# Performance work log

Hardware: AMD Instinct MI355X
Metric: run time of the kernel (lower is better)

Reference implementation:

```python
import jax, jax.numpy as jnp
import numpy as np

N = 50000       # nodes
E = 1600000     # edges (before self-loops)
NFEAT = 256
NHID = 8        # hidden units per head
HEADS = 8
NCLASS = 16
L1 = 0.5        # damping lambda layer 1
L2 = 0.5        # damping lambda layer 2
SLOPE = 0.2     # LeakyReLU negative slope (PyG GATConv default)


def setup_inputs() -> dict:
    ks = jax.random.split(jax.random.key(0), 16)
    g = lambda k, shape, fan: jax.random.normal(k, shape, jnp.float32) * (1.0 / np.sqrt(fan))
    return {
        "x": jax.random.normal(ks[0], (N, NFEAT), jnp.float32),
        "edge_index": jax.random.randint(ks[1], (2, E), 0, N, jnp.int64),
        # conv1: GATConv(nfeat -> nhid, heads=HEADS, concat=True)
        "W1": g(ks[2], (NFEAT, HEADS * NHID), NFEAT),
        "a1_src": g(ks[3], (HEADS, NHID), NHID),
        "a1_dst": g(ks[4], (HEADS, NHID), NHID),
        "b1": jnp.zeros((HEADS * NHID,), jnp.float32),
        # conv2: GATConv(nhid*heads -> nclass, heads=1, concat=False)
        "W2": g(ks[5], (HEADS * NHID, NCLASS), HEADS * NHID),
        "a2_src": g(ks[6], (1, NCLASS), NCLASS),
        "a2_dst": g(ks[7], (1, NCLASS), NCLASS),
        "b2": jnp.zeros((NCLASS,), jnp.float32),
        # side-branch linear layers
        "fc1_W": g(ks[8], (NFEAT, NHID), NFEAT),
        "fc1_b": jnp.zeros((NHID,), jnp.float32),
        "fc2_W": g(ks[9], (HEADS * NHID, NCLASS), HEADS * NHID),
        "fc2_b": jnp.zeros((NCLASS,), jnp.float32),
    }


def gat_conv(x, W, a_src, a_dst, b, src, dst, heads, outc, concat):
    n = x.shape[0]
    h = (x @ W).reshape(n, heads, outc)                 # [N, H, C]
    alpha_s = jnp.sum(h * a_src, axis=-1)               # [N, H]
    alpha_d = jnp.sum(h * a_dst, axis=-1)               # [N, H]
    e = jax.nn.leaky_relu(alpha_s[src] + alpha_d[dst], SLOPE)  # [Etot, H]
    # segment softmax over incoming edges of each destination node
    m = jax.ops.segment_max(e, dst, num_segments=n)
    m = jax.lax.stop_gradient(m)                        # max-shift is grad-neutral
    ex = jnp.exp(e - m[dst])
    denom = jax.ops.segment_sum(ex, dst, num_segments=n)
    alpha = ex / denom[dst]                             # [Etot, H]
    out = jax.ops.segment_sum(h[src] * alpha[:, :, None], dst, num_segments=n)
    if concat:
        out = out.reshape(n, heads * outc)
    else:
        out = out.mean(axis=1)
    return out + b


def reference(x, edge_index, W1, a1_src, a1_dst, b1, W2, a2_src, a2_dst, b2,
              fc1_W, fc1_b, fc2_W, fc2_b):
    loop = jnp.arange(N, dtype=edge_index.dtype)
    src = jnp.concatenate([edge_index[0], loop])
    dst = jnp.concatenate([edge_index[1], loop])
    # layer 1: GATConv + damped linear side branch
    out1 = gat_conv(x, W1, a1_src, a1_dst, b1, src, dst, HEADS, NHID, True)
    side1 = jnp.tile(x @ fc1_W + fc1_b, (1, HEADS))     # cat of heads copies
    h = jax.nn.elu(out1 - L1 * side1)                   # [N, H*C]
    # layer 2
    out2 = gat_conv(h, W2, a2_src, a2_dst, b2, src, dst, 1, NCLASS, False)
    side2 = h @ fc2_W + fc2_b
    return jax.nn.log_softmax(out2 - L2 * side2, axis=1)
```

## Files before the change

kernel.cpp:

```cpp
#include <hip/hip_runtime.h>
#include <hip/hip_bf16.h>
#include <cstddef>

constexpr int N      = 50000;
constexpr int E      = 1600000;
constexpr int NFEAT  = 256;
constexpr float SLOPE = 0.2f;
constexpr float L1d  = 0.5f;
constexpr float L2d  = 0.5f;

constexpr int BSHIFT = 7;
constexpr int NBUK   = (N + 127) >> BSHIFT;
constexpr int EPB    = 4096;
constexpr int NBLK   = (E + EPB - 1) / EPB;
constexpr int CAP    = 5120;

constexpr size_t al64(size_t x) { return (x + 63) & ~size_t(63); }
constexpr size_t W_OFFS  = 0;
constexpr size_t W_CSR   = W_OFFS  + al64(N + 1);
constexpr size_t W_STAGE = W_CSR   + (size_t)E;
constexpr size_t W_BHIST = W_STAGE + (size_t)E;
constexpr size_t W_TOT   = W_BHIST + al64((size_t)NBLK * NBUK);
constexpr size_t W_BBASE = W_TOT   + al64(NBUK);
constexpr size_t W_H1B   = W_BBASE + al64(NBUK + 1);
constexpr size_t W_S1B   = W_H1B   + (size_t)N * 32;
constexpr size_t W_D1    = W_S1B   + (size_t)N * 4;
constexpr size_t W_SIDE1 = W_D1    + (size_t)N * 8;
constexpr size_t W_HF    = W_SIDE1 + (size_t)N * 8;
constexpr size_t W_H2B   = W_HF    + (size_t)N * 64;
constexpr size_t W_SIDE2 = W_H2B   + (size_t)N * 8;
constexpr size_t W_S2B   = W_SIDE2 + (size_t)N * 16;
constexpr size_t W_D2    = W_S2B   + al64(N / 2);

typedef short bf16x8 __attribute__((ext_vector_type(8)));
typedef float f32x4  __attribute__((ext_vector_type(4)));

__device__ inline short f2bf(float f) {
    unsigned u = __builtin_bit_cast(unsigned, f);
    u += 0x7FFF + ((u >> 16) & 1);
    return (short)(u >> 16);
}


__global__ __launch_bounds__(256) void p1_hist_kernel(const int* __restrict__ ei,
                                                      int* __restrict__ bhist) {
    __shared__ int hist[NBUK];
    int tid = threadIdx.x;
    for (int j = tid; j < NBUK; j += 256) hist[j] = 0;
    __syncthreads();
    int base = blockIdx.x * EPB;
    int end = base + EPB; if (end > E) end = E;
    for (int i = base + tid; i < end; i += 256) {
        int d = ei[E + i];
        atomicAdd(&hist[d >> BSHIFT], 1);
    }
    __syncthreads();
    for (int j = tid; j < NBUK; j += 256) bhist[(size_t)blockIdx.x * NBUK + j] = hist[j];
}

__global__ __launch_bounds__(512) void s1_scan_kernel(int* __restrict__ bhist,
                                                      int* __restrict__ tot) {
    __shared__ int sd[512];
    int tid = threadIdx.x;
    int b = blockIdx.x;
    int v = (tid < NBLK) ? bhist[(size_t)tid * NBUK + b] : 0;
    sd[tid] = v;
    __syncthreads();
    for (int off = 1; off < 512; off <<= 1) {
        int t = (tid >= off) ? sd[tid - off] : 0;
        __syncthreads();
        sd[tid] += t;
        __syncthreads();
    }
    if (tid < NBLK) bhist[(size_t)tid * NBUK + b] = sd[tid] - v;
    if (tid == 511) tot[b] = sd[511];
}

__global__ __launch_bounds__(512) void s2_scan_kernel(const int* __restrict__ tot,
                                                      int* __restrict__ bbase,
                                                      int* __restrict__ offs) {
    __shared__ int sd[512];
    int tid = threadIdx.x;
    int v = (tid < NBUK) ? tot[tid] : 0;
    sd[tid] = v;
    __syncthreads();
    for (int off = 1; off < 512; off <<= 1) {
        int t = (tid >= off) ? sd[tid - off] : 0;
        __syncthreads();
        sd[tid] += t;
        __syncthreads();
    }
    if (tid < NBUK) bbase[tid] = sd[tid] - v;
    if (tid == 0) { bbase[NBUK] = E; offs[N] = E; }
}

__global__ __launch_bounds__(256) void p2_stage_kernel(const int* __restrict__ ei,
                                                       const int* __restrict__ bhist,
                                                       const int* __restrict__ bbase,
                                                       unsigned int* __restrict__ stage) {
    __shared__ int cur[NBUK];
    int tid = threadIdx.x;
    for (int j = tid; j < NBUK; j += 256)
        cur[j] = bbase[j] + bhist[(size_t)blockIdx.x * NBUK + j];
    __syncthreads();
    int base = blockIdx.x * EPB;
    int end = base + EPB; if (end > E) end = E;
    for (int i = base + tid; i < end; i += 256) {
        int s = ei[i];
        int d = ei[E + i];
        int b = d >> BSHIFT;
        int pos = atomicAdd(&cur[b], 1);
        stage[pos] = ((unsigned int)(d & 127) << 24) | (unsigned int)s;
    }
}

__global__ __launch_bounds__(256) void p3_fine_kernel(const unsigned int* __restrict__ stage,
                                                      const int* __restrict__ bbase,
                                                      int* __restrict__ offs,
                                                      int* __restrict__ csr) {
    __shared__ unsigned int sstage[CAP];
    __shared__ int hist[128];
    __shared__ int scn[128];
    __shared__ int cur[128];
    int tid = threadIdx.x;
    int b = blockIdx.x;
    int ebase = bbase[b], eend = bbase[b + 1];
    int cnt = eend - ebase;
    if (tid < 128) hist[tid] = 0;
    __syncthreads();
    for (int i = tid; i < cnt; i += 256) {
        unsigned int p = stage[ebase + i];
        if (i < CAP) sstage[i] = p;
        atomicAdd(&hist[p >> 24], 1);
    }
    __syncthreads();
    if (tid < 128) scn[tid] = hist[tid];
    __syncthreads();
    for (int off = 1; off < 128; off <<= 1) {
        int t = (tid < 128 && tid >= off) ? scn[tid - off] : 0;
        __syncthreads();
        if (tid < 128) scn[tid] += t;
        __syncthreads();
    }
    if (tid < 128) {
        int excl = scn[tid] - hist[tid];
        cur[tid] = excl;
        int v = (b << BSHIFT) + tid;
        if (v < N) offs[v] = ebase + excl;
    }
    __syncthreads();
    for (int i = tid; i < cnt; i += 256) {
        unsigned int p = (i < CAP) ? sstage[i] : stage[ebase + i];
        int dloc = (int)(p >> 24);
        int s = (int)(p & 0xFFFFFFu);
        int r = atomicAdd(&cur[dloc], 1);
        csr[ebase + r] = s;
    }
}

__global__ __launch_bounds__(256) void gemm1_kernel(const float* __restrict__ x,
                                                    const float* __restrict__ W1,
                                                    const float* __restrict__ fc1W,
                                                    const float* __restrict__ fc1b,
                                                    short* __restrict__ h1b,
                                                    float* __restrict__ side1) {
    __shared__ bf16x8 wfrag[2560];
    int tid = threadIdx.x;

    for (int s = tid; s < 2560; s += 256) {
        int l = s & 63;
        int t = s >> 6;
        int nt = t % 5, kt = t / 5;
        int col = nt * 16 + (l & 15);
        int kbase = kt * 32 + (l >> 4) * 8;
        bf16x8 v;
#pragma unroll
        for (int j = 0; j < 8; ++j) {
            float f = 0.f;
            if (col < 64)      f = W1[(size_t)(kbase + j) * 64 + col];
            else if (col < 72) f = fc1W[(size_t)(kbase + j) * 8 + (col - 64)];
            v[j] = f2bf(f);
        }
        wfrag[s] = v;
    }
    __syncthreads();

    int w = tid >> 6;
    int l = tid & 63;
    int row0 = blockIdx.x * 64;
    int arow = row0 + w * 16 + (l & 15);
    if (arow >= N) arow = N - 1;
    const float* ap = x + (size_t)arow * NFEAT + ((l >> 4) * 8);

    f32x4 acc[5];
#pragma unroll
    for (int nt = 0; nt < 5; ++nt) acc[nt] = (f32x4){0.f, 0.f, 0.f, 0.f};

#pragma unroll
    for (int kt = 0; kt < 8; ++kt) {
        float4 alo = *reinterpret_cast<const float4*>(ap + kt * 32);
        float4 ahi = *reinterpret_cast<const float4*>(ap + kt * 32 + 4);
        bf16x8 af;
        af[0] = f2bf(alo.x); af[1] = f2bf(alo.y); af[2] = f2bf(alo.z); af[3] = f2bf(alo.w);
        af[4] = f2bf(ahi.x); af[5] = f2bf(ahi.y); af[6] = f2bf(ahi.z); af[7] = f2bf(ahi.w);
#pragma unroll
        for (int nt = 0; nt < 5; ++nt) {
            acc[nt] = __builtin_amdgcn_mfma_f32_16x16x32_bf16(
                af, wfrag[(kt * 5 + nt) * 64 + l], acc[nt], 0, 0, 0);
        }
    }

    int cbase = l & 15;
    int rbase = row0 + w * 16 + (l >> 4) * 4;
#pragma unroll
    for (int nt = 0; nt < 4; ++nt) {
#pragma unroll
        for (int r = 0; r < 4; ++r) {
            int row = rbase + r;
            if (row < N) h1b[(size_t)row * 64 + nt * 16 + cbase] = f2bf(acc[nt][r]);
        }
    }
    if (cbase < 8) {
        float bb = fc1b[cbase];
#pragma unroll
        for (int r = 0; r < 4; ++r) {
            int row = rbase + r;
            if (row < N) side1[(size_t)row * 8 + cbase] = acc[4][r] + bb;
        }
    }
}

__global__ __launch_bounds__(256) void alpha1_kernel(const __hip_bfloat16* __restrict__ h1b,
                                                     const float* __restrict__ a1s,
                                                     const float* __restrict__ a1d,
                                                     __hip_bfloat16* __restrict__ s1b,
                                                     float* __restrict__ d1) {
    int wave = threadIdx.x >> 6;
    int lane = threadIdx.x & 63;
    int v = blockIdx.x * 4 + wave;
    if (v >= N) return;
    float hv = __bfloat162float(h1b[(size_t)v * 64 + lane]);
    float sa = hv * a1s[lane];
    float sd = hv * a1d[lane];
#pragma unroll
    for (int off = 1; off < 8; off <<= 1) {
        sa += __shfl_xor(sa, off, 64);
        sd += __shfl_xor(sd, off, 64);
    }
    if ((lane & 7) == 0) {
        s1b[v * 8 + (lane >> 3)] = __float2bfloat16(sa);
        d1[v * 8 + (lane >> 3)] = sd;
    }
}

__global__ __launch_bounds__(256) void agg1_kernel(const int* __restrict__ offs,
                                                   const int* __restrict__ csr,
                                                   const __hip_bfloat16* __restrict__ h1b,
                                                   const __hip_bfloat16* __restrict__ s1b,
                                                   const float* __restrict__ d1,
                                                   const float* __restrict__ side1,
                                                   const float* __restrict__ b1,
                                                   float* __restrict__ hf) {
    int wave = threadIdx.x >> 6;
    int lane = threadIdx.x & 63;
    int v = blockIdx.x * 4 + wave;
    if (v >= N) return;
    int j  = lane >> 3;
    int hh = lane & 7;
    int hc = lane >> 3;

    float dv_att = d1[v * 8 + hh];
    float dv_ch  = __shfl(dv_att, hc, 64);

    float e0 = __bfloat162float(s1b[v * 8 + hc]) + dv_ch;
    e0 = fmaxf(e0, SLOPE * e0);
    float ex0 = __expf(e0);
    float acc = ex0 * __bfloat162float(h1b[(size_t)v * 64 + lane]);
    float den_ch = ex0;
    float den_att = 0.f;

    int beg = offs[v], end = offs[v + 1];
    int nfull = (end - beg) >> 3;
    int i = beg;
    for (int g = 0; g < nfull; ++g, i += 8) {
        int s = csr[i + j];
        float a = __bfloat162float(s1b[s * 8 + hh]) + dv_att;
        a = fmaxf(a, SLOPE * a);
        float xv = __expf(a);
        den_att += xv;
#pragma unroll
        for (int jj = 0; jj < 8; ++jj) {
            int sj = __builtin_amdgcn_readlane(s, jj * 8);
            float xj = __shfl(xv, jj * 8 + hc, 64);
            const __hip_bfloat16* hp = h1b + ((size_t)sj << 6);
            acc += xj * __bfloat162float(hp[lane]);
        }
    }
    for (; i < end; ++i) {
        int s = csr[i];
        float a = __bfloat162float(s1b[s * 8 + hc]) + dv_ch;
        a = fmaxf(a, SLOPE * a);
        float x = __expf(a);
        acc += x * __bfloat162float(h1b[(size_t)s * 64 + lane]);
        den_ch += x;
    }

    den_att += __shfl_xor(den_att, 8, 64);
    den_att += __shfl_xor(den_att, 16, 64);
    den_att += __shfl_xor(den_att, 32, 64);
    float den = den_ch + __shfl(den_att, hc, 64);

    float o = acc / den + b1[lane];
    float z = o - L1d * side1[v * 8 + (lane & 7)];
    hf[(size_t)v * 64 + lane] = z > 0.f ? z : (__expf(z) - 1.f);
}

__global__ __launch_bounds__(256) void gemm2_kernel(const float* __restrict__ hf,
                                                    const float* __restrict__ W2,
                                                    const float* __restrict__ fc2W,
                                                    const float* __restrict__ fc2b,
                                                    __hip_bfloat16* __restrict__ h2b,
                                                    float* __restrict__ side2) {
    __shared__ float xs[128][65];
    __shared__ float ws[64][33];
    int tid = threadIdx.x;
    int ty = tid >> 3;
    int tx = tid & 7;
    int row0 = blockIdx.x * 128;

    float acc[4][4];
#pragma unroll
    for (int i = 0; i < 4; ++i)
#pragma unroll
        for (int j = 0; j < 4; ++j) acc[i][j] = 0.f;

    int lr = tid >> 4;
    int lj = tid & 15;
#pragma unroll
    for (int it = 0; it < 8; ++it) {
        int r = lr + it * 16;
        int grow = row0 + r;
        if (grow >= N) grow = N - 1;
        float4 vv = *reinterpret_cast<const float4*>(&hf[(size_t)grow * 64 + lj * 4]);
        xs[r][lj * 4 + 0] = vv.x;
        xs[r][lj * 4 + 1] = vv.y;
        xs[r][lj * 4 + 2] = vv.z;
        xs[r][lj * 4 + 3] = vv.w;
    }
    for (int idx = tid; idx < 64 * 32; idx += 256) {
        int k = idx >> 5;
        int c = idx & 31;
        float v = (c < 16) ? W2[(size_t)k * 16 + c] : fc2W[(size_t)k * 16 + (c - 16)];
        ws[k][c] = v;
    }
    __syncthreads();
#pragma unroll 4
    for (int k = 0; k < 64; ++k) {
        float xv[4], wv[4];
#pragma unroll
        for (int i = 0; i < 4; ++i) xv[i] = xs[ty * 4 + i][k];
#pragma unroll
        for (int j = 0; j < 4; ++j) wv[j] = ws[k][tx * 4 + j];
#pragma unroll
        for (int i = 0; i < 4; ++i)
#pragma unroll
            for (int j = 0; j < 4; ++j) acc[i][j] += xv[i] * wv[j];
    }

#pragma unroll
    for (int i = 0; i < 4; ++i) {
        int row = row0 + ty * 4 + i;
        if (row >= N) continue;
#pragma unroll
        for (int j = 0; j < 4; ++j) {
            int c = tx * 4 + j;
            if (c < 16) h2b[(size_t)row * 16 + c] = __float2bfloat16(acc[i][j]);
            else        side2[(size_t)row * 16 + (c - 16)] = acc[i][j] + fc2b[c - 16];
        }
    }
}

__global__ __launch_bounds__(256) void alpha2_kernel(const __hip_bfloat16* __restrict__ h2b,
                                                     const float* __restrict__ a2s,
                                                     const float* __restrict__ a2d,
                                                     __hip_bfloat16* __restrict__ s2b,
                                                     float* __restrict__ d2) {
    int wave = threadIdx.x >> 6;
    int lane = threadIdx.x & 63;
    int vbase = (blockIdx.x * 4 + wave) * 4;
    int r = lane >> 4;
    int c = lane & 15;
    int v = vbase + r;
    float hv = (v < N) ? __bfloat162float(h2b[(size_t)v * 16 + c]) : 0.f;
    float sa = hv * a2s[c];
    float sd = hv * a2d[c];
#pragma unroll
    for (int off = 1; off < 16; off <<= 1) {
        sa += __shfl_xor(sa, off, 64);
        sd += __shfl_xor(sd, off, 64);
    }
    if (v < N && c == 0) {
        s2b[v] = __float2bfloat16(sa);
        d2[v] = sd;
    }
}

__global__ __launch_bounds__(256) void agg2_kernel(const int* __restrict__ offs,
                                                   const int* __restrict__ csr,
                                                   const __hip_bfloat16* __restrict__ h2b,
                                                   const __hip_bfloat16* __restrict__ s2b,
                                                   const float* __restrict__ d2,
                                                   const float* __restrict__ side2,
                                                   const float* __restrict__ b2,
                                                   float* __restrict__ out) {
    int wave = threadIdx.x >> 6;
    int lane = threadIdx.x & 63;
    int v = blockIdx.x * 4 + wave;
    if (v >= N) return;
    int c = lane & 15;
    int slot = lane >> 4;
    float dv = d2[v];

    float acc = 0.f, den = 0.f;
    if (slot == 0) {
        float e = __bfloat162float(s2b[v]) + dv;
        e = e > 0.f ? e : SLOPE * e;
        float ex = __expf(e);
        acc = ex * __bfloat162float(h2b[(size_t)v * 16 + c]);
        den = ex;
    }
    int beg = offs[v], end = offs[v + 1];
    int i = beg + slot;
    for (; i + 4 < end; i += 8) {
        int sA = csr[i];
        int sB = csr[i + 4];
        float aA = __bfloat162float(s2b[sA]);
        float aB = __bfloat162float(s2b[sB]);
        float hA = __bfloat162float(h2b[(size_t)sA * 16 + c]);
        float hB = __bfloat162float(h2b[(size_t)sB * 16 + c]);
        aA += dv; aA = aA > 0.f ? aA : SLOPE * aA; float xA = __expf(aA);
        aB += dv; aB = aB > 0.f ? aB : SLOPE * aB; float xB = __expf(aB);
        acc += xA * hA; den += xA;
        acc += xB * hB; den += xB;
    }
    if (i < end) {
        int s = csr[i];
        float a = __bfloat162float(s2b[s]) + dv;
        a = a > 0.f ? a : SLOPE * a;
        float x = __expf(a);
        acc += x * __bfloat162float(h2b[(size_t)s * 16 + c]);
        den += x;
    }
    acc += __shfl_xor(acc, 16, 64);
    acc += __shfl_xor(acc, 32, 64);
    den += __shfl_xor(den, 16, 64);
    den += __shfl_xor(den, 32, 64);

    float o = acc / den + b2[c];
    float z = o - L2d * side2[(size_t)v * 16 + c];

    float m = z;
#pragma unroll
    for (int off = 1; off < 16; off <<= 1) m = fmaxf(m, __shfl_xor(m, off, 64));
    float ex = __expf(z - m);
    float s = ex;
#pragma unroll
    for (int off = 1; off < 16; off <<= 1) s += __shfl_xor(s, off, 64);
    float lsm = z - m - __logf(s);
    if (slot == 0) out[(size_t)v * 16 + c] = lsm;
}

extern "C" void kernel_launch(void* const* d_in, const int* in_sizes, int n_in,
                              void* d_out, int out_size, void* d_ws, size_t ws_size,
                              hipStream_t stream) {
    const float* x    = (const float*)d_in[0];
    const int*   ei   = (const int*)d_in[1];
    const float* W1   = (const float*)d_in[2];
    const float* a1s  = (const float*)d_in[3];
    const float* a1d  = (const float*)d_in[4];
    const float* b1   = (const float*)d_in[5];
    const float* W2   = (const float*)d_in[6];
    const float* a2s  = (const float*)d_in[7];
    const float* a2d  = (const float*)d_in[8];
    const float* b2   = (const float*)d_in[9];
    const float* fc1W = (const float*)d_in[10];
    const float* fc1b = (const float*)d_in[11];
    const float* fc2W = (const float*)d_in[12];
    const float* fc2b = (const float*)d_in[13];
    float* out = (float*)d_out;

    int*   wsi = (int*)d_ws;
    float* wsf = (float*)d_ws;
    int*   offs   = wsi + W_OFFS;
    int*   csr    = wsi + W_CSR;
    unsigned int* stage = (unsigned int*)(wsi + W_STAGE);
    int*   bhist  = wsi + W_BHIST;
    int*   tot    = wsi + W_TOT;
    int*   bbase  = wsi + W_BBASE;
    __hip_bfloat16* h1b = (__hip_bfloat16*)(wsf + W_H1B);
    __hip_bfloat16* s1b = (__hip_bfloat16*)(wsf + W_S1B);
    float* d1     = wsf + W_D1;
    float* side1  = wsf + W_SIDE1;
    float* hf     = wsf + W_HF;
    __hip_bfloat16* h2b = (__hip_bfloat16*)(wsf + W_H2B);
    float* side2  = wsf + W_SIDE2;
    __hip_bfloat16* s2b = (__hip_bfloat16*)(wsf + W_S2B);
    float* d2     = wsf + W_D2;

    p1_hist_kernel<<<NBLK, 256, 0, stream>>>(ei, bhist);
    s1_scan_kernel<<<NBUK, 512, 0, stream>>>(bhist, tot);
    s2_scan_kernel<<<1, 512, 0, stream>>>(tot, bbase, offs);
    p2_stage_kernel<<<NBLK, 256, 0, stream>>>(ei, bhist, bbase, stage);
    p3_fine_kernel<<<NBUK, 256, 0, stream>>>(stage, bbase, offs, csr);

    gemm1_kernel<<<(N + 63) / 64, 256, 0, stream>>>(x, W1, fc1W, fc1b,
                                                    (short*)h1b, side1);
    alpha1_kernel<<<(N + 3) / 4, 256, 0, stream>>>(h1b, a1s, a1d, s1b, d1);
    agg1_kernel<<<(N + 3) / 4, 256, 0, stream>>>(offs, csr, h1b, s1b, d1, side1, b1, hf);

    gemm2_kernel<<<(N + 127) / 128, 256, 0, stream>>>(hf, W2, fc2W, fc2b, h2b, side2);
    alpha2_kernel<<<(N + 15) / 16, 256, 0, stream>>>(h2b, a2s, a2d, s2b, d2);
    agg2_kernel<<<(N + 3) / 4, 256, 0, stream>>>(offs, csr, h2b, s2b, d2, side2, b2, out);
}
```

Before: 171.8 us.

## Software-pipeline neighbor gathers in both aggregation kernels with clamped masked groups

Result: faster. 156.7 us (-8.8%).

```diff
diff --git a/kernel.cpp b/kernel.cpp
--- a/kernel.cpp
+++ b/kernel.cpp
@@ -41,6 +41,10 @@
     return (short)(u >> 16);
 }
 
+__device__ inline float bfu2f(unsigned short u) {
+    return __builtin_bit_cast(float, (unsigned)u << 16);
+}
+
 
 __global__ __launch_bounds__(256) void p1_hist_kernel(const int* __restrict__ ei,
                                                       int* __restrict__ bhist) {
@@ -255,8 +259,8 @@
 
 __global__ __launch_bounds__(256) void agg1_kernel(const int* __restrict__ offs,
                                                    const int* __restrict__ csr,
-                                                   const __hip_bfloat16* __restrict__ h1b,
-                                                   const __hip_bfloat16* __restrict__ s1b,
+                                                   const unsigned short* __restrict__ h1u,
+                                                   const unsigned short* __restrict__ s1u,
                                                    const float* __restrict__ d1,
                                                    const float* __restrict__ side1,
                                                    const float* __restrict__ b1,
@@ -272,43 +276,102 @@
     float dv_att = d1[v * 8 + hh];
     float dv_ch  = __shfl(dv_att, hc, 64);
 
-    float e0 = __bfloat162float(s1b[v * 8 + hc]) + dv_ch;
+    float e0 = bfu2f(s1u[v * 8 + hc]) + dv_ch;
     e0 = fmaxf(e0, SLOPE * e0);
     float ex0 = __expf(e0);
-    float acc = ex0 * __bfloat162float(h1b[(size_t)v * 64 + lane]);
-    float den_ch = ex0;
+    float acc = ex0 * bfu2f(h1u[(size_t)v * 64 + lane]);
+    float den0 = ex0;
     float den_att = 0.f;
 
     int beg = offs[v], end = offs[v + 1];
-    int nfull = (end - beg) >> 3;
-    int i = beg;
-    for (int g = 0; g < nfull; ++g, i += 8) {
-        int s = csr[i + j];
-        float a = __bfloat162float(s1b[s * 8 + hh]) + dv_att;
+    int deg = end - beg;
+    int ng = (deg + 7) >> 3;
+
+    auto csrg = [&](int g) {
+        int idx = beg + g * 8 + j;
+        idx = idx < end - 1 ? idx : end - 1;
+        idx = idx > 0 ? idx : 0;
+        return csr[idx];
+    };
+
+    unsigned short hA[8], hB[8];
+    int sA = 0, sB = 0;
+    float svA = 0.f, svB = 0.f;
+
+    if (ng > 0) {
+        sA = csrg(0);
+        svA = bfu2f(s1u[sA * 8 + hh]);
+#pragma unroll
+        for (int jj = 0; jj < 8; ++jj) {
+            int sj = __builtin_amdgcn_readlane(sA, jj * 8);
+            const unsigned short* p = h1u + ((size_t)sj << 6);
+            hA[jj] = p[lane];
+        }
+        sB = csrg(1);
+    }
+
+    int g = 0;
+    for (; g + 1 < ng; g += 2) {
+        svB = bfu2f(s1u[sB * 8 + hh]);
+#pragma unroll
+        for (int jj = 0; jj < 8; ++jj) {
+            int sj = __builtin_amdgcn_readlane(sB, jj * 8);
+            const unsigned short* p = h1u + ((size_t)sj << 6);
+            hB[jj] = p[lane];
+        }
+        int sC = csrg(g + 2);
+        {
+            float a = svA + dv_att;
+            a = fmaxf(a, SLOPE * a);
+            float xv = __expf(a);
+            xv = (beg + g * 8 + j < end) ? xv : 0.f;
+            den_att += xv;
+#pragma unroll
+            for (int jj = 0; jj < 8; ++jj) {
+                float xj = __shfl(xv, jj * 8 + hc, 64);
+                acc += xj * bfu2f(hA[jj]);
+            }
+        }
+        sA = sC;
+        svA = bfu2f(s1u[sA * 8 + hh]);
+#pragma unroll
+        for (int jj = 0; jj < 8; ++jj) {
+            int sj = __builtin_amdgcn_readlane(sA, jj * 8);
+            const unsigned short* p = h1u + ((size_t)sj << 6);
+            hA[jj] = p[lane];
+        }
+        int sD = csrg(g + 3);
+        {
+            float a = svB + dv_att;
+            a = fmaxf(a, SLOPE * a);
+            float xv = __expf(a);
+            xv = (beg + (g + 1) * 8 + j < end) ? xv : 0.f;
+            den_att += xv;
+#pragma unroll
+            for (int jj = 0; jj < 8; ++jj) {
+                float xj = __shfl(xv, jj * 8 + hc, 64);
+                acc += xj * bfu2f(hB[jj]);
+            }
+        }
+        sB = sD;
+    }
+    if (g < ng) {
+        float a = svA + dv_att;
         a = fmaxf(a, SLOPE * a);
         float xv = __expf(a);
+        xv = (beg + g * 8 + j < end) ? xv : 0.f;
         den_att += xv;
 #pragma unroll
         for (int jj = 0; jj < 8; ++jj) {
-            int sj = __builtin_amdgcn_readlane(s, jj * 8);
             float xj = __shfl(xv, jj * 8 + hc, 64);
-            const __hip_bfloat16* hp = h1b + ((size_t)sj << 6);
-            acc += xj * __bfloat162float(hp[lane]);
-        }
-    }
-    for (; i < end; ++i) {
-        int s = csr[i];
-        float a = __bfloat162float(s1b[s * 8 + hc]) + dv_ch;
-        a = fmaxf(a, SLOPE * a);
-        float x = __expf(a);
-        acc += x * __bfloat162float(h1b[(size_t)s * 64 + lane]);
-        den_ch += x;
+            acc += xj * bfu2f(hA[jj]);
+        }
     }
 
     den_att += __shfl_xor(den_att, 8, 64);
     den_att += __shfl_xor(den_att, 16, 64);
     den_att += __shfl_xor(den_att, 32, 64);
-    float den = den_ch + __shfl(den_att, hc, 64);
+    float den = den0 + __shfl(den_att, hc, 64);
 
     float o = acc / den + b1[lane];
     float z = o - L1d * side1[v * 8 + (lane & 7)];
@@ -407,8 +470,8 @@
 
 __global__ __launch_bounds__(256) void agg2_kernel(const int* __restrict__ offs,
                                                    const int* __restrict__ csr,
-                                                   const __hip_bfloat16* __restrict__ h2b,
-                                                   const __hip_bfloat16* __restrict__ s2b,
+                                                   const unsigned short* __restrict__ h2u,
+                                                   const unsigned short* __restrict__ s2u,
                                                    const float* __restrict__ d2,
                                                    const float* __restrict__ side2,
                                                    const float* __restrict__ b2,
@@ -423,34 +486,67 @@
 
     float acc = 0.f, den = 0.f;
     if (slot == 0) {
-        float e = __bfloat162float(s2b[v]) + dv;
-        e = e > 0.f ? e : SLOPE * e;
+        float e = bfu2f(s2u[v]) + dv;
+        e = fmaxf(e, SLOPE * e);
         float ex = __expf(e);
-        acc = ex * __bfloat162float(h2b[(size_t)v * 16 + c]);
+        acc = ex * bfu2f(h2u[(size_t)v * 16 + c]);
         den = ex;
     }
     int beg = offs[v], end = offs[v + 1];
-    int i = beg + slot;
-    for (; i + 4 < end; i += 8) {
-        int sA = csr[i];
-        int sB = csr[i + 4];
-        float aA = __bfloat162float(s2b[sA]);
-        float aB = __bfloat162float(s2b[sB]);
-        float hA = __bfloat162float(h2b[(size_t)sA * 16 + c]);
-        float hB = __bfloat162float(h2b[(size_t)sB * 16 + c]);
-        aA += dv; aA = aA > 0.f ? aA : SLOPE * aA; float xA = __expf(aA);
-        aB += dv; aB = aB > 0.f ? aB : SLOPE * aB; float xB = __expf(aB);
-        acc += xA * hA; den += xA;
-        acc += xB * hB; den += xB;
-    }
-    if (i < end) {
-        int s = csr[i];
-        float a = __bfloat162float(s2b[s]) + dv;
-        a = a > 0.f ? a : SLOPE * a;
+    int deg = end - beg;
+    int ng = (deg + 3) >> 2;
+
+    auto csrg = [&](int g) {
+        int idx = beg + g * 4 + slot;
+        idx = idx < end - 1 ? idx : end - 1;
+        idx = idx > 0 ? idx : 0;
+        return csr[idx];
+    };
+
+    int sA = 0, sB = 0;
+    float svA = 0.f, svB = 0.f, hvA = 0.f, hvB = 0.f;
+    if (ng > 0) {
+        sA = csrg(0);
+        svA = bfu2f(s2u[sA]);
+        hvA = bfu2f(h2u[(size_t)sA * 16 + c]);
+        sB = csrg(1);
+    }
+    int g = 0;
+    for (; g + 1 < ng; g += 2) {
+        svB = bfu2f(s2u[sB]);
+        hvB = bfu2f(h2u[(size_t)sB * 16 + c]);
+        int sC = csrg(g + 2);
+        {
+            float a = svA + dv;
+            a = fmaxf(a, SLOPE * a);
+            float x = __expf(a);
+            x = (beg + g * 4 + slot < end) ? x : 0.f;
+            acc += x * hvA;
+            den += x;
+        }
+        sA = sC;
+        svA = bfu2f(s2u[sA]);
+        hvA = bfu2f(h2u[(size_t)sA * 16 + c]);
+        int sD = csrg(g + 3);
+        {
+            float a = svB + dv;
+            a = fmaxf(a, SLOPE * a);
+            float x = __expf(a);
+            x = (beg + (g + 1) * 4 + slot < end) ? x : 0.f;
+            acc += x * hvB;
+            den += x;
+        }
+        sB = sD;
+    }
+    if (g < ng) {
+        float a = svA + dv;
+        a = fmaxf(a, SLOPE * a);
         float x = __expf(a);
-        acc += x * __bfloat162float(h2b[(size_t)s * 16 + c]);
+        x = (beg + g * 4 + slot < end) ? x : 0.f;
+        acc += x * hvA;
         den += x;
     }
+
     acc += __shfl_xor(acc, 16, 64);
     acc += __shfl_xor(acc, 32, 64);
     den += __shfl_xor(den, 16, 64);
@@ -516,9 +612,15 @@
     gemm1_kernel<<<(N + 63) / 64, 256, 0, stream>>>(x, W1, fc1W, fc1b,
                                                     (short*)h1b, side1);
     alpha1_kernel<<<(N + 3) / 4, 256, 0, stream>>>(h1b, a1s, a1d, s1b, d1);
-    agg1_kernel<<<(N + 3) / 4, 256, 0, stream>>>(offs, csr, h1b, s1b, d1, side1, b1, hf);
+    agg1_kernel<<<(N + 3) / 4, 256, 0, stream>>>(offs, csr,
+                                                 (const unsigned short*)h1b,
+                                                 (const unsigned short*)s1b,
+                                                 d1, side1, b1, hf);
 
     gemm2_kernel<<<(N + 127) / 128, 256, 0, stream>>>(hf, W2, fc2W, fc2b, h2b, side2);
     alpha2_kernel<<<(N + 15) / 16, 256, 0, stream>>>(h2b, a2s, a2d, s2b, d2);
-    agg2_kernel<<<(N + 3) / 4, 256, 0, stream>>>(offs, csr, h2b, s2b, d2, side2, b2, out);
-}
+    agg2_kernel<<<(N + 3) / 4, 256, 0, stream>>>(offs, csr,
+                                                 (const unsigned short*)h2b,
+                                                 (const unsigned short*)s2b,
+                                                 d2, side2, b2, out);
+}
```

## Software-pipeline neighbor gathers in both aggregation kernels with swizzle-based broadcasts

Applied to the files above, without the earlier changes.

After: 171.0 us. Within noise of the previous version (-0.4%).

```diff
diff --git a/kernel.cpp b/kernel.cpp
--- a/kernel.cpp
+++ b/kernel.cpp
@@ -41,6 +41,12 @@
     return (short)(u >> 16);
 }
 
+__device__ inline float bfu2f(unsigned short u) {
+    return __builtin_bit_cast(float, (unsigned)u << 16);
+}
+
+#define SWZ8(x, PAT) __builtin_bit_cast(float, __builtin_amdgcn_ds_swizzle(__builtin_bit_cast(int, (x)), (PAT)))
+
 
 __global__ __launch_bounds__(256) void p1_hist_kernel(const int* __restrict__ ei,
                                                       int* __restrict__ bhist) {
@@ -255,63 +261,127 @@
 
 __global__ __launch_bounds__(256) void agg1_kernel(const int* __restrict__ offs,
                                                    const int* __restrict__ csr,
-                                                   const __hip_bfloat16* __restrict__ h1b,
-                                                   const __hip_bfloat16* __restrict__ s1b,
+                                                   const unsigned short* __restrict__ h1u,
+                                                   const unsigned short* __restrict__ s1u,
                                                    const float* __restrict__ d1,
                                                    const float* __restrict__ side1,
                                                    const float* __restrict__ b1,
                                                    float* __restrict__ hf) {
-    int wave = threadIdx.x >> 6;
     int lane = threadIdx.x & 63;
-    int v = blockIdx.x * 4 + wave;
+    int v = blockIdx.x * 4 + (threadIdx.x >> 6);
     if (v >= N) return;
-    int j  = lane >> 3;
-    int hh = lane & 7;
-    int hc = lane >> 3;
-
-    float dv_att = d1[v * 8 + hh];
-    float dv_ch  = __shfl(dv_att, hc, 64);
-
-    float e0 = __bfloat162float(s1b[v * 8 + hc]) + dv_ch;
+    int j  = lane & 7;
+    int hh = lane >> 3;
+
+    float dv = d1[v * 8 + hh];
+
+    float e0 = bfu2f(s1u[v * 8 + hh]) + dv;
     e0 = fmaxf(e0, SLOPE * e0);
     float ex0 = __expf(e0);
-    float acc = ex0 * __bfloat162float(h1b[(size_t)v * 64 + lane]);
-    float den_ch = ex0;
+    float acc = ex0 * bfu2f(h1u[(size_t)v * 64 + lane]);
+    float den0 = ex0;
     float den_att = 0.f;
 
     int beg = offs[v], end = offs[v + 1];
-    int nfull = (end - beg) >> 3;
-    int i = beg;
-    for (int g = 0; g < nfull; ++g, i += 8) {
-        int s = csr[i + j];
-        float a = __bfloat162float(s1b[s * 8 + hh]) + dv_att;
+    int deg = end - beg;
+    int ngf = deg >> 3;
+    int rem = deg & 7;
+
+    const int* cb = csr + beg;
+
+    unsigned short hA[8], hB[8];
+    int s8A = 0, s8B = 0;
+    float svA = 0.f, svB = 0.f;
+
+#define LOADH(s8, h)                                                        \
+    do {                                                                     \
+        int sj0 = __builtin_amdgcn_readlane(s8, 0);                          \
+        int sj1 = __builtin_amdgcn_readlane(s8, 1);                          \
+        int sj2 = __builtin_amdgcn_readlane(s8, 2);                          \
+        int sj3 = __builtin_amdgcn_readlane(s8, 3);                          \
+        int sj4 = __builtin_amdgcn_readlane(s8, 4);                          \
+        int sj5 = __builtin_amdgcn_readlane(s8, 5);                          \
+        int sj6 = __builtin_amdgcn_readlane(s8, 6);                          \
+        int sj7 = __builtin_amdgcn_readlane(s8, 7);                          \
+        h[0] = h1u[((size_t)sj0 << 6) + lane];                               \
+        h[1] = h1u[((size_t)sj1 << 6) + lane];                               \
+        h[2] = h1u[((size_t)sj2 << 6) + lane];                               \
+        h[3] = h1u[((size_t)sj3 << 6) + lane];                               \
+        h[4] = h1u[((size_t)sj4 << 6) + lane];                               \
+        h[5] = h1u[((size_t)sj5 << 6) + lane];                               \
+        h[6] = h1u[((size_t)sj6 << 6) + lane];                               \
+        h[7] = h1u[((size_t)sj7 << 6) + lane];                               \
+    } while (0)
+
+#define COMP(sv, h)                                                          \
+    do {                                                                     \
+        float a = (sv) + dv;                                                 \
+        a = fmaxf(a, SLOPE * a);                                             \
+        float xv = __expf(a);                                                \
+        den_att += xv;                                                       \
+        acc += SWZ8(xv, 0x018) * bfu2f(h[0]);                                \
+        acc += SWZ8(xv, 0x038) * bfu2f(h[1]);                                \
+        acc += SWZ8(xv, 0x058) * bfu2f(h[2]);                                \
+        acc += SWZ8(xv, 0x078) * bfu2f(h[3]);                                \
+        acc += SWZ8(xv, 0x098) * bfu2f(h[4]);                                \
+        acc += SWZ8(xv, 0x0B8) * bfu2f(h[5]);                                \
+        acc += SWZ8(xv, 0x0D8) * bfu2f(h[6]);                                \
+        acc += SWZ8(xv, 0x0F8) * bfu2f(h[7]);                                \
+    } while (0)
+
+    if (ngf > 0) {
+        s8A = cb[j];
+        svA = bfu2f(s1u[s8A * 8 + hh]);
+        LOADH(s8A, hA);
+        if (ngf > 1) s8B = cb[8 + j];
+    }
+    int g = 0;
+    for (; g + 1 < ngf; g += 2) {
+        svB = bfu2f(s1u[s8B * 8 + hh]);
+        LOADH(s8B, hB);
+        int s8C = (g + 2 < ngf) ? cb[(g + 2) * 8 + j] : 0;
+        COMP(svA, hA);
+        s8A = s8C;
+        if (g + 2 < ngf) {
+            svA = bfu2f(s1u[s8A * 8 + hh]);
+            LOADH(s8A, hA);
+        }
+        int s8D = (g + 3 < ngf) ? cb[(g + 3) * 8 + j] : 0;
+        COMP(svB, hB);
+        s8B = s8D;
+    }
+    if (g < ngf) COMP(svA, hA);
+
+    if (rem) {
+        int idx = beg + ngf * 8 + j;
+        idx = idx < end ? idx : end - 1;
+        int s8 = csr[idx];
+        float a = bfu2f(s1u[s8 * 8 + hh]) + dv;
         a = fmaxf(a, SLOPE * a);
         float xv = __expf(a);
+        xv = (j < rem) ? xv : 0.f;
         den_att += xv;
-#pragma unroll
-        for (int jj = 0; jj < 8; ++jj) {
-            int sj = __builtin_amdgcn_readlane(s, jj * 8);
-            float xj = __shfl(xv, jj * 8 + hc, 64);
-            const __hip_bfloat16* hp = h1b + ((size_t)sj << 6);
-            acc += xj * __bfloat162float(hp[lane]);
-        }
-    }
-    for (; i < end; ++i) {
-        int s = csr[i];
-        float a = __bfloat162float(s1b[s * 8 + hc]) + dv_ch;
-        a = fmaxf(a, SLOPE * a);
-        float x = __expf(a);
-        acc += x * __bfloat162float(h1b[(size_t)s * 64 + lane]);
-        den_ch += x;
-    }
-
-    den_att += __shfl_xor(den_att, 8, 64);
-    den_att += __shfl_xor(den_att, 16, 64);
-    den_att += __shfl_xor(den_att, 32, 64);
-    float den = den_ch + __shfl(den_att, hc, 64);
+        unsigned short ht[8];
+        LOADH(s8, ht);
+        acc += SWZ8(xv, 0x018) * bfu2f(ht[0]);
+        acc += SWZ8(xv, 0x038) * bfu2f(ht[1]);
+        acc += SWZ8(xv, 0x058) * bfu2f(ht[2]);
+        acc += SWZ8(xv, 0x078) * bfu2f(ht[3]);
+        acc += SWZ8(xv, 0x098) * bfu2f(ht[4]);
+        acc += SWZ8(xv, 0x0B8) * bfu2f(ht[5]);
+        acc += SWZ8(xv, 0x0D8) * bfu2f(ht[6]);
+        acc += SWZ8(xv, 0x0F8) * bfu2f(ht[7]);
+    }
+#undef LOADH
+#undef COMP
+
+    den_att += __shfl_xor(den_att, 1, 64);
+    den_att += __shfl_xor(den_att, 2, 64);
+    den_att += __shfl_xor(den_att, 4, 64);
+    float den = den0 + den_att;
 
     float o = acc / den + b1[lane];
-    float z = o - L1d * side1[v * 8 + (lane & 7)];
+    float z = o - L1d * side1[v * 8 + j];
     hf[(size_t)v * 64 + lane] = z > 0.f ? z : (__expf(z) - 1.f);
 }
 
@@ -407,50 +477,85 @@
 
 __global__ __launch_bounds__(256) void agg2_kernel(const int* __restrict__ offs,
                                                    const int* __restrict__ csr,
-                                                   const __hip_bfloat16* __restrict__ h2b,
-                                                   const __hip_bfloat16* __restrict__ s2b,
+                                                   const unsigned short* __restrict__ h2u,
+                                                   const unsigned short* __restrict__ s2u,
                                                    const float* __restrict__ d2,
                                                    const float* __restrict__ side2,
                                                    const float* __restrict__ b2,
                                                    float* __restrict__ out) {
-    int wave = threadIdx.x >> 6;
     int lane = threadIdx.x & 63;
-    int v = blockIdx.x * 4 + wave;
+    int v = blockIdx.x * 4 + (threadIdx.x >> 6);
     if (v >= N) return;
     int c = lane & 15;
     int slot = lane >> 4;
+    int j4 = lane & 3;
+    int slotaddr = slot << 2;
     float dv = d2[v];
 
     float acc = 0.f, den = 0.f;
     if (slot == 0) {
-        float e = __bfloat162float(s2b[v]) + dv;
-        e = e > 0.f ? e : SLOPE * e;
+        float e = bfu2f(s2u[v]) + dv;
+        e = fmaxf(e, SLOPE * e);
         float ex = __expf(e);
-        acc = ex * __bfloat162float(h2b[(size_t)v * 16 + c]);
+        acc = ex * bfu2f(h2u[(size_t)v * 16 + c]);
         den = ex;
     }
     int beg = offs[v], end = offs[v + 1];
-    int i = beg + slot;
-    for (; i + 4 < end; i += 8) {
-        int sA = csr[i];
-        int sB = csr[i + 4];
-        float aA = __bfloat162float(s2b[sA]);
-        float aB = __bfloat162float(s2b[sB]);
-        float hA = __bfloat162float(h2b[(size_t)sA * 16 + c]);
-        float hB = __bfloat162float(h2b[(size_t)sB * 16 + c]);
-        aA += dv; aA = aA > 0.f ? aA : SLOPE * aA; float xA = __expf(aA);
-        aB += dv; aB = aB > 0.f ? aB : SLOPE * aB; float xB = __expf(aB);
-        acc += xA * hA; den += xA;
-        acc += xB * hB; den += xB;
-    }
-    if (i < end) {
-        int s = csr[i];
-        float a = __bfloat162float(s2b[s]) + dv;
-        a = a > 0.f ? a : SLOPE * a;
-        float x = __expf(a);
-        acc += x * __bfloat162float(h2b[(size_t)s * 16 + c]);
-        den += x;
-    }
+    int deg = end - beg;
+    int ngf = deg >> 2;
+    int rem = deg & 3;
+    const int* cb = csr + beg;
+
+#define COMP2(s4, sv)                                                        \
+    do {                                                                     \
+        float a = (sv) + dv;                                                 \
+        a = fmaxf(a, SLOPE * a);                                             \
+        float xv = __expf(a);                                                \
+        float xs = __builtin_bit_cast(float,                                 \
+            __builtin_amdgcn_ds_bpermute(slotaddr, __builtin_bit_cast(int, xv))); \
+        int ss = __builtin_amdgcn_ds_bpermute(slotaddr, (s4));               \
+        float hv = bfu2f(h2u[((size_t)ss << 4) + c]);                        \
+        acc += xs * hv;                                                      \
+        den += xs;                                                           \
+    } while (0)
+
+    int s4A = 0, s4B = 0;
+    float svA = 0.f, svB = 0.f;
+    if (ngf > 0) {
+        s4A = cb[j4];
+        svA = bfu2f(s2u[s4A]);
+        if (ngf > 1) s4B = cb[4 + j4];
+    }
+    int g = 0;
+    for (; g + 1 < ngf; g += 2) {
+        svB = bfu2f(s2u[s4B]);
+        int s4C = (g + 2 < ngf) ? cb[(g + 2) * 4 + j4] : 0;
+        COMP2(s4A, svA);
+        s4A = s4C;
+        if (g + 2 < ngf) svA = bfu2f(s2u[s4A]);
+        int s4D = (g + 3 < ngf) ? cb[(g + 3) * 4 + j4] : 0;
+        COMP2(s4B, svB);
+        s4B = s4D;
+    }
+    if (g < ngf) COMP2(s4A, svA);
+
+    if (rem) {
+        int idx = beg + ngf * 4 + j4;
+        idx = idx < end ? idx : end - 1;
+        int s4 = csr[idx];
+        float a = bfu2f(s2u[s4]) + dv;
+        a = fmaxf(a, SLOPE * a);
+        float xv = __expf(a);
+        xv = (j4 < rem) ? xv : 0.f;
+        float xs = __builtin_bit_cast(float,
+            __builtin_amdgcn_ds_bpermute(slotaddr, __builtin_bit_cast(int, xv)));
+        int ss = __builtin_amdgcn_ds_bpermute(slotaddr, s4);
+        float hv = bfu2f(h2u[((size_t)ss << 4) + c]);
+        acc += xs * hv;
+        den += xs;
+    }
+#undef COMP2
+
     acc += __shfl_xor(acc, 16, 64);
     acc += __shfl_xor(acc, 32, 64);
     den += __shfl_xor(den, 16, 64);
@@ -516,9 +621,15 @@
     gemm1_kernel<<<(N + 63) / 64, 256, 0, stream>>>(x, W1, fc1W, fc1b,
                                                     (short*)h1b, side1);
     alpha1_kernel<<<(N + 3) / 4, 256, 0, stream>>>(h1b, a1s, a1d, s1b, d1);
-    agg1_kernel<<<(N + 3) / 4, 256, 0, stream>>>(offs, csr, h1b, s1b, d1, side1, b1, hf);
+    agg1_kernel<<<(N + 3) / 4, 256, 0, stream>>>(offs, csr,
+                                                 (const unsigned short*)h1b,
+                                                 (const unsigned short*)s1b,
+                                                 d1, side1, b1, hf);
 
     gemm2_kernel<<<(N + 127) / 128, 256, 0, stream>>>(hf, W2, fc2W, fc2b, h2b, side2);
     alpha2_kernel<<<(N + 15) / 16, 256, 0, stream>>>(h2b, a2s, a2d, s2b, d2);
-    agg2_kernel<<<(N + 3) / 4, 256, 0, stream>>>(offs, csr, h2b, s2b, d2, side2, b2, out);
-}
+    agg2_kernel<<<(N + 3) / 4, 256, 0, stream>>>(offs, csr,
+                                                 (const unsigned short*)h2b,
+                                                 (const unsigned short*)s2b,
+                                                 d2, side2, b2, out);
+}
```
